# Kernel optimization log

Measured on AMD Instinct MI355X. Metric: run time of the kernel, lower is better.

The kernel has to match this reference:

```python
import jax, jax.numpy as jnp
import numpy as np

B, C, W, H = 4, 256, 64, 64
D = C // 8  # reduced query/key channels


def setup_inputs() -> dict:
    key = jax.random.key(0)
    k1, k2, k3, k4, k5 = jax.random.split(key, 5)
    return {
        "x": jax.random.normal(k1, (B, C, W, H), dtype=jnp.float32),
        "q_weight": jax.random.normal(k2, (D, C), dtype=jnp.float32) * 0.05,
        "k_weight": jax.random.normal(k3, (D, C), dtype=jnp.float32) * 0.05,
        "v_weight": jax.random.normal(k4, (C, C), dtype=jnp.float32) * 0.05,
        "gamma": jax.random.normal(k5, (1,), dtype=jnp.float32),
    }


def reference(x, q_weight, k_weight, v_weight, gamma):
    b, c, w, h = x.shape
    n = w * h
    xf = x.reshape(b, c, n)                       # (B, C, N)
    # 1x1 convs == channel matmuls
    q = jnp.einsum('dc,bcn->bdn', q_weight, xf)   # (B, D, N)
    k = jnp.einsum('dc,bcn->bdn', k_weight, xf)   # (B, D, N)
    v = jnp.einsum('oc,bcn->bon', v_weight, xf)   # (B, C, N)
    # energy[b, i, j] = <q[:, i], k[:, j]>  (unscaled, single head)
    energy = jnp.einsum('bdi,bdj->bij', q, k)     # (B, N, N)
    attn = jax.nn.softmax(energy, axis=-1)        # softmax over keys j
    # out[b, c, i] = sum_j v[b, c, j] * attn[b, i, j]
    out = jnp.einsum('bcj,bij->bci', v, attn)     # (B, C, N)
    out = out.reshape(b, c, w, h)
    return gamma[0] * out + x
```

## Files before the change

kernel.cpp:

```cpp
#include <hip/hip_runtime.h>
#include <math.h>

#define Bb 4
#define Cc 256
#define Nn 4096
#define Dd 32
#define XST 264

typedef __attribute__((ext_vector_type(8))) short bf16x8;
typedef __attribute__((ext_vector_type(4))) float f32x4;

__device__ __forceinline__ unsigned short f2bf(float x) {
    union { float f; unsigned u; } c; c.f = x;
    unsigned r = c.u + 0x7fffu + ((c.u >> 16) & 1u);
    return (unsigned short)(r >> 16);
}
__device__ __forceinline__ unsigned pk2(float a, float b) {
    return (unsigned)f2bf(a) | ((unsigned)f2bf(b) << 16);
}
__device__ __forceinline__ float fexp2(float x) {
#if __has_builtin(__builtin_amdgcn_exp2f)
    return __builtin_amdgcn_exp2f(x);
#else
    return __exp2f(x);
#endif
}
__device__ __forceinline__ void wg_barrier() {
    asm volatile("s_waitcnt lgkmcnt(0)\n\ts_barrier" ::: "memory");
}
template <int CTRL>
__device__ __forceinline__ float dppf(float v) {
    int iv = __builtin_bit_cast(int, v);
    return __builtin_bit_cast(float,
        __builtin_amdgcn_update_dpp(iv, iv, CTRL, 0xF, 0xF, false));
}
__device__ __forceinline__ float rowsum16(float v) {
    v += dppf<0xB1>(v);
    v += dppf<0x4E>(v);
    v += dppf<0x141>(v);
    v += dppf<0x140>(v);
    return v;
}

__global__ __launch_bounds__(256) void pack_w(
    const float* __restrict__ qw, const float* __restrict__ kw,
    const float* __restrict__ vw, short* __restrict__ wpk) {
    const int g = blockIdx.x * 256 + threadIdx.x;
    const int qd = g & 3, m = (g >> 2) & 15, kc = (g >> 6) & 7, ot = g >> 9;
    const int o = 16 * ot + m;
    const float* src;
    float scale = 1.0f;
    if (o < 32)      { src = qw + (size_t)o * Cc; scale = 1.44269504088896f; }
    else if (o < 64) { src = kw + (size_t)(o - 32) * Cc; }
    else             { src = vw + (size_t)(o - 64) * Cc; }
    const float* s8 = src + 32 * kc + 8 * qd;
    uint4 u;
    u.x = pk2(s8[0] * scale, s8[1] * scale);
    u.y = pk2(s8[2] * scale, s8[3] * scale);
    u.z = pk2(s8[4] * scale, s8[5] * scale);
    u.w = pk2(s8[6] * scale, s8[7] * scale);
    *(uint4*)(wpk + (size_t)g * 8) = u;
}

__global__ __launch_bounds__(256) void proj(
    const float* __restrict__ x, const short* __restrict__ wpk,
    short* __restrict__ q_t, short* __restrict__ k_t, short* __restrict__ v_b) {
    __shared__ alignas(16) short xs[32 * XST];
    const int b = blockIdx.z;
    const int n0 = blockIdx.x * 32;
    const int tid = threadIdx.x;
    const int w = tid >> 6;
    const int lane = tid & 63, qd = lane >> 4, m = lane & 15;

    {
        const int n = tid & 31, cg = tid >> 5;
        const float* xp = x + ((size_t)b * Cc + 32 * cg) * Nn + n0 + n;
        float xv[32];
#pragma unroll
        for (int i = 0; i < 32; ++i) xv[i] = xp[(size_t)i * Nn];
        short* row = xs + n * XST + 32 * cg;
#pragma unroll
        for (int u4 = 0; u4 < 4; ++u4)
            *(uint4*)(row + 8 * u4) = make_uint4(
                pk2(xv[8*u4+0], xv[8*u4+1]), pk2(xv[8*u4+2], xv[8*u4+3]),
                pk2(xv[8*u4+4], xv[8*u4+5]), pk2(xv[8*u4+6], xv[8*u4+7]));
    }
    __syncthreads();

    const int fslot = m * 4 + qd;
    f32x4 acc[5][2];
#pragma unroll
    for (int i = 0; i < 5; ++i)
#pragma unroll
        for (int nt = 0; nt < 2; ++nt) acc[i][nt] = (f32x4){0.f, 0.f, 0.f, 0.f};

    bf16x8 afc[5], afn[5];
#pragma unroll
    for (int i = 0; i < 5; ++i)
        afc[i] = *(const bf16x8*)(wpk + ((size_t)((4*i + w) * 8 + 0) * 64 + fslot) * 8);

    for (int kc = 0; kc < 8; ++kc) {
        if (kc < 7) {
#pragma unroll
            for (int i = 0; i < 5; ++i)
                afn[i] = *(const bf16x8*)(
                    wpk + ((size_t)((4*i + w) * 8 + kc + 1) * 64 + fslot) * 8);
        }
        const bf16x8 b0 = *(const bf16x8*)&xs[(     m) * XST + 32 * kc + 8 * qd];
        const bf16x8 b1 = *(const bf16x8*)&xs[(16 + m) * XST + 32 * kc + 8 * qd];
#pragma unroll
        for (int i = 0; i < 5; ++i)
            acc[i][0] = __builtin_amdgcn_mfma_f32_16x16x32_bf16(afc[i], b0, acc[i][0], 0, 0, 0);
#pragma unroll
        for (int i = 0; i < 5; ++i)
            acc[i][1] = __builtin_amdgcn_mfma_f32_16x16x32_bf16(afc[i], b1, acc[i][1], 0, 0, 0);
#pragma unroll
        for (int i = 0; i < 5; ++i) afc[i] = afn[i];
    }

#pragma unroll
    for (int i = 0; i < 5; ++i) {
        const int ot = 4 * i + w;
        if (ot < 4) {
            short* dst = (ot < 2 ? q_t : k_t) + (size_t)b * Nn * Dd;
            const int dbase = (ot & 1) * 16 + 4 * qd;
#pragma unroll
            for (int nt = 0; nt < 2; ++nt) {
                const f32x4 a = acc[i][nt];
                *(uint2*)(dst + (size_t)(n0 + 16 * nt + m) * Dd + dbase) =
                    make_uint2(pk2(a[0], a[1]), pk2(a[2], a[3]));
            }
        } else {
            const int ct = ot - 4;
            const int jt = n0 >> 6;
            const int b5 = (n0 >> 5) & 1;
            const size_t vbase =
                (((size_t)(b * 64 + jt) * 32 + ct * 2 + (m >> 3)) * 64
                 + ((m >> 1) & 3) * 16 + 4 * qd) * 8 + 4 * (m & 1) + 2 * b5;
#pragma unroll
            for (int rr = 0; rr < 4; ++rr) {
                const unsigned pv = pk2(acc[i][0][rr], acc[i][1][rr]);
                *(unsigned*)(v_b + vbase + rr * 8) = pv;
            }
        }
    }
}

__global__ __launch_bounds__(512) void attn(
    const float* __restrict__ x, const short* __restrict__ q_t,
    const short* __restrict__ k_t, const short* __restrict__ v_b,
    const float* __restrict__ gamma, float* __restrict__ out) {
    __shared__ alignas(16) char pool[34304];
    float* l_s = (float*)(pool + 33792);
    float* o_t = (float*)pool;

    const int fb  = blockIdx.x;
    const int xcd = fb & 7;
    const int b   = xcd >> 1;
    const int i0  = (((xcd & 1) << 5) | (fb >> 3)) << 6;
    const int tid = threadIdx.x;
    const int w = tid >> 6, lane = tid & 63;
    const int qd = lane >> 4, m = lane & 15;
    const int rt = w & 3, kh = w >> 2;

    const bf16x8 af = *(const bf16x8*)(
        q_t + ((size_t)b * Nn + i0 + 16 * rt + m) * Dd + 8 * qd);

    const short* kf = k_t + (size_t)b * Nn * Dd + (32 * kh + m) * Dd + 8 * qd;
    const short* vw = v_b + (size_t)b * (64 * 32 * 64 * 8) + (4 * w) * 512 + lane * 8;

    bf16x8 bkA0 = *(const bf16x8*)(kf);
    bf16x8 bkA1 = *(const bf16x8*)(kf + 512);
    bf16x8 bkB0 = *(const bf16x8*)(kf + 2048);
    bf16x8 bkB1 = *(const bf16x8*)(kf + 2560);
    bf16x8 vfA[2][2], vfB[2][2];
#pragma unroll
    for (int ct = 0; ct < 2; ++ct)
#pragma unroll
        for (int kc = 0; kc < 2; ++kc)
            vfA[ct][kc] = *(const bf16x8*)(vw + (2 * ct + kc) * 512);

    f32x4 oacc[4][2];
#pragma unroll
    for (int mt = 0; mt < 4; ++mt)
#pragma unroll
        for (int ct = 0; ct < 2; ++ct) oacc[mt][ct] = (f32x4){0.f, 0.f, 0.f, 0.f};
    float l_i[4] = {0.f, 0.f, 0.f, 0.f};

    const short* kpre = kf + 4096;
    const short* vpre = vw + 16384;

    for (int j2 = 0; j2 < 32; ++j2) {
        const bool pre = (j2 < 31);
        {
            short* ps = (short*)pool;
            const f32x4 s0 = __builtin_amdgcn_mfma_f32_16x16x32_bf16(
                af, bkA0, (f32x4){0.f, 0.f, 0.f, 0.f}, 0, 0, 0);
            const f32x4 s1 = __builtin_amdgcn_mfma_f32_16x16x32_bf16(
                af, bkA1, (f32x4){0.f, 0.f, 0.f, 0.f}, 0, 0, 0);
            if (pre) {
                bkA0 = *(const bf16x8*)(kpre);
                bkA1 = *(const bf16x8*)(kpre + 512);
            }
#pragma unroll
            for (int rr = 0; rr < 4; ++rr) {
                const float p0 = fexp2(s0[rr]);
                const float p1 = fexp2(s1[rr]);
                l_i[rr] += p0 + p1;
                *(unsigned*)&ps[(16 * rt + 4 * qd + rr) * 72 + 4 * m + 2 * kh] =
                    pk2(p0, p1);
            }
            wg_barrier();
#pragma unroll
            for (int ct = 0; ct < 2; ++ct)
#pragma unroll
                for (int kc = 0; kc < 2; ++kc)
                    vfB[ct][kc] = *(const bf16x8*)(vpre + (2 * ct + kc) * 512);
            __builtin_amdgcn_s_setprio(1);
#pragma unroll
            for (int kc = 0; kc < 2; ++kc) {
                bf16x8 pa[4];
#pragma unroll
                for (int mt = 0; mt < 4; ++mt)
                    pa[mt] = *(const bf16x8*)&ps[(16 * mt + m) * 72 + 32 * kc + 8 * qd];
#pragma unroll
                for (int ct = 0; ct < 2; ++ct)
#pragma unroll
                    for (int mt = 0; mt < 4; ++mt)
                        oacc[mt][ct] = __builtin_amdgcn_mfma_f32_16x16x32_bf16(
                            pa[mt], vfA[ct][kc], oacc[mt][ct], 0, 0, 0);
            }
            __builtin_amdgcn_s_setprio(0);
        }
        {
            short* ps = (short*)(pool + 9216);
            const f32x4 s0 = __builtin_amdgcn_mfma_f32_16x16x32_bf16(
                af, bkB0, (f32x4){0.f, 0.f, 0.f, 0.f}, 0, 0, 0);
            const f32x4 s1 = __builtin_amdgcn_mfma_f32_16x16x32_bf16(
                af, bkB1, (f32x4){0.f, 0.f, 0.f, 0.f}, 0, 0, 0);
            if (pre) {
                bkB0 = *(const bf16x8*)(kpre + 2048);
                bkB1 = *(const bf16x8*)(kpre + 2560);
            }
#pragma unroll
            for (int rr = 0; rr < 4; ++rr) {
                const float p0 = fexp2(s0[rr]);
                const float p1 = fexp2(s1[rr]);
                l_i[rr] += p0 + p1;
                *(unsigned*)&ps[(16 * rt + 4 * qd + rr) * 72 + 4 * m + 2 * kh] =
                    pk2(p0, p1);
            }
            wg_barrier();
            if (pre) {
#pragma unroll
                for (int ct = 0; ct < 2; ++ct)
#pragma unroll
                    for (int kc = 0; kc < 2; ++kc)
                        vfA[ct][kc] = *(const bf16x8*)(vpre + 16384 + (2 * ct + kc) * 512);
            }
            __builtin_amdgcn_s_setprio(1);
#pragma unroll
            for (int kc = 0; kc < 2; ++kc) {
                bf16x8 pa[4];
#pragma unroll
                for (int mt = 0; mt < 4; ++mt)
                    pa[mt] = *(const bf16x8*)&ps[(16 * mt + m) * 72 + 32 * kc + 8 * qd];
#pragma unroll
                for (int ct = 0; ct < 2; ++ct)
#pragma unroll
                    for (int mt = 0; mt < 4; ++mt)
                        oacc[mt][ct] = __builtin_amdgcn_mfma_f32_16x16x32_bf16(
                            pa[mt], vfB[ct][kc], oacc[mt][ct], 0, 0, 0);
            }
            __builtin_amdgcn_s_setprio(0);
        }
        kpre += 4096;
        vpre += 32768;
    }

#pragma unroll
    for (int rr = 0; rr < 4; ++rr) l_i[rr] = rowsum16(l_i[rr]);
    if (m == 0)
        *(f32x4*)&l_s[kh * 64 + 16 * rt + 4 * qd] =
            (f32x4){l_i[0], l_i[1], l_i[2], l_i[3]};
    __syncthreads();

    const float g = gamma[0];
    const int i = tid & 63, cg8 = tid >> 6;
    const float linv = 1.0f / (l_s[i] + l_s[64 + i]);
#pragma unroll
    for (int ps = 0; ps < 2; ++ps) {
        if (ps) __syncthreads();
#pragma unroll
        for (int mt = 0; mt < 4; ++mt)
#pragma unroll
            for (int rr = 0; rr < 4; ++rr)
                o_t[(16 * mt + 4 * qd + rr) * 132 + 16 * w + m] = oacc[mt][ps][rr];
        __syncthreads();
#pragma unroll
        for (int u = 0; u < 4; ++u) {
            const f32x4 v4 = *(const f32x4*)&o_t[i * 132 + 16 * cg8 + 4 * u];
#pragma unroll
            for (int e = 0; e < 4; ++e) {
                const int c = 32 * cg8 + 16 * ps + 4 * u + e;
                const size_t gidx = ((size_t)b * Cc + c) * Nn + i0 + i;
                out[gidx] = g * v4[e] * linv + x[gidx];
            }
        }
    }
}

extern "C" void kernel_launch(void* const* d_in, const int* in_sizes, int n_in,
                              void* d_out, int out_size, void* d_ws, size_t ws_size,
                              hipStream_t stream) {
    const float* x     = (const float*)d_in[0];
    const float* qw    = (const float*)d_in[1];
    const float* kw    = (const float*)d_in[2];
    const float* vw    = (const float*)d_in[3];
    const float* gamma = (const float*)d_in[4];
    float* out = (float*)d_out;

    short* q_t = (short*)d_ws;
    short* k_t = q_t + (size_t)Bb * Nn * Dd;
    short* v_b = k_t + (size_t)Bb * Nn * Dd;
    short* wpk = v_b + (size_t)Bb * Cc * Nn;

    pack_w<<<dim3(40), 256, 0, stream>>>(qw, kw, vw, wpk);
    proj<<<dim3(Nn / 32, 1, Bb), 256, 0, stream>>>(x, wpk, q_t, k_t, v_b);
    attn<<<dim3(256), 512, 0, stream>>>(x, q_t, k_t, v_b, gamma, out);
}
```

Before: 135.8 us.

## Split attention output channels across two blocks to double grid parallelism

The attention kernel now launches 512 blocks instead of 256. Each block handles 64 query rows and half of the 256 value channels, so each wave keeps one channel tile of accumulators instead of two. This halves per-block PV work and register use (launch bounds now request 4 blocks per SM), which should fill the 256 CUs better. In exchange, QK^T and the softmax exponentials are computed twice per query tile, and K is loaded by both halves.

```diff
diff --git a/kernel.cpp b/kernel.cpp
--- a/kernel.cpp
+++ b/kernel.cpp
@@ -146,7 +146,7 @@
     }
 }
 
-__global__ __launch_bounds__(512) void attn(
+__global__ __launch_bounds__(512, 4) void attn(
     const float* __restrict__ x, const short* __restrict__ q_t,
     const short* __restrict__ k_t, const short* __restrict__ v_b,
     const float* __restrict__ gamma, float* __restrict__ out) {
@@ -154,10 +154,11 @@
     float* l_s = (float*)(pool + 33792);
     float* o_t = (float*)pool;
 
-    const int fb  = blockIdx.x;
-    const int xcd = fb & 7;
-    const int b   = xcd >> 1;
-    const int i0  = (((xcd & 1) << 5) | (fb >> 3)) << 6;
+    const int fb   = blockIdx.x;
+    const int xcd  = fb & 7;
+    const int b    = xcd >> 1;
+    const int half = xcd & 1;
+    const int i0   = (fb >> 3) << 6;
     const int tid = threadIdx.x;
     const int w = tid >> 6, lane = tid & 63;
     const int qd = lane >> 4, m = lane & 15;
@@ -167,24 +168,21 @@
         q_t + ((size_t)b * Nn + i0 + 16 * rt + m) * Dd + 8 * qd);
 
     const short* kf = k_t + (size_t)b * Nn * Dd + (32 * kh + m) * Dd + 8 * qd;
-    const short* vw = v_b + (size_t)b * (64 * 32 * 64 * 8) + (4 * w) * 512 + lane * 8;
+    const short* vw = v_b + (size_t)b * (64 * 32 * 64 * 8)
+                    + (size_t)(16 * half + 2 * w) * 512 + lane * 8;
 
     bf16x8 bkA0 = *(const bf16x8*)(kf);
     bf16x8 bkA1 = *(const bf16x8*)(kf + 512);
     bf16x8 bkB0 = *(const bf16x8*)(kf + 2048);
     bf16x8 bkB1 = *(const bf16x8*)(kf + 2560);
-    bf16x8 vfA[2][2], vfB[2][2];
-#pragma unroll
-    for (int ct = 0; ct < 2; ++ct)
-#pragma unroll
-        for (int kc = 0; kc < 2; ++kc)
-            vfA[ct][kc] = *(const bf16x8*)(vw + (2 * ct + kc) * 512);
-
-    f32x4 oacc[4][2];
-#pragma unroll
-    for (int mt = 0; mt < 4; ++mt)
-#pragma unroll
-        for (int ct = 0; ct < 2; ++ct) oacc[mt][ct] = (f32x4){0.f, 0.f, 0.f, 0.f};
+    bf16x8 vfA[2], vfB[2];
+#pragma unroll
+    for (int kc = 0; kc < 2; ++kc)
+        vfA[kc] = *(const bf16x8*)(vw + kc * 512);
+
+    f32x4 oacc[4];
+#pragma unroll
+    for (int mt = 0; mt < 4; ++mt) oacc[mt] = (f32x4){0.f, 0.f, 0.f, 0.f};
     float l_i[4] = {0.f, 0.f, 0.f, 0.f};
 
     const short* kpre = kf + 4096;
@@ -212,10 +210,8 @@
             }
             wg_barrier();
 #pragma unroll
-            for (int ct = 0; ct < 2; ++ct)
-#pragma unroll
-                for (int kc = 0; kc < 2; ++kc)
-                    vfB[ct][kc] = *(const bf16x8*)(vpre + (2 * ct + kc) * 512);
+            for (int kc = 0; kc < 2; ++kc)
+                vfB[kc] = *(const bf16x8*)(vpre + kc * 512);
             __builtin_amdgcn_s_setprio(1);
 #pragma unroll
             for (int kc = 0; kc < 2; ++kc) {
@@ -224,11 +220,9 @@
                 for (int mt = 0; mt < 4; ++mt)
                     pa[mt] = *(const bf16x8*)&ps[(16 * mt + m) * 72 + 32 * kc + 8 * qd];
 #pragma unroll
-                for (int ct = 0; ct < 2; ++ct)
-#pragma unroll
-                    for (int mt = 0; mt < 4; ++mt)
-                        oacc[mt][ct] = __builtin_amdgcn_mfma_f32_16x16x32_bf16(
-                            pa[mt], vfA[ct][kc], oacc[mt][ct], 0, 0, 0);
+                for (int mt = 0; mt < 4; ++mt)
+                    oacc[mt] = __builtin_amdgcn_mfma_f32_16x16x32_bf16(
+                        pa[mt], vfA[kc], oacc[mt], 0, 0, 0);
             }
             __builtin_amdgcn_s_setprio(0);
         }
@@ -253,10 +247,8 @@
             wg_barrier();
             if (pre) {
 #pragma unroll
-                for (int ct = 0; ct < 2; ++ct)
-#pragma unroll
-                    for (int kc = 0; kc < 2; ++kc)
-                        vfA[ct][kc] = *(const bf16x8*)(vpre + 16384 + (2 * ct + kc) * 512);
+                for (int kc = 0; kc < 2; ++kc)
+                    vfA[kc] = *(const bf16x8*)(vpre + 16384 + kc * 512);
             }
             __builtin_amdgcn_s_setprio(1);
 #pragma unroll
@@ -266,11 +258,9 @@
                 for (int mt = 0; mt < 4; ++mt)
                     pa[mt] = *(const bf16x8*)&ps[(16 * mt + m) * 72 + 32 * kc + 8 * qd];
 #pragma unroll
-                for (int ct = 0; ct < 2; ++ct)
-#pragma unroll
-                    for (int mt = 0; mt < 4; ++mt)
-                        oacc[mt][ct] = __builtin_amdgcn_mfma_f32_16x16x32_bf16(
-                            pa[mt], vfB[ct][kc], oacc[mt][ct], 0, 0, 0);
+                for (int mt = 0; mt < 4; ++mt)
+                    oacc[mt] = __builtin_amdgcn_mfma_f32_16x16x32_bf16(
+                        pa[mt], vfB[kc], oacc[mt], 0, 0, 0);
             }
             __builtin_amdgcn_s_setprio(0);
         }
@@ -286,23 +276,21 @@
     __syncthreads();
 
     const float g = gamma[0];
-    const int i = tid & 63, cg8 = tid >> 6;
-    const float linv = 1.0f / (l_s[i] + l_s[64 + i]);
-#pragma unroll
-    for (int ps = 0; ps < 2; ++ps) {
-        if (ps) __syncthreads();
-#pragma unroll
-        for (int mt = 0; mt < 4; ++mt)
-#pragma unroll
-            for (int rr = 0; rr < 4; ++rr)
-                o_t[(16 * mt + 4 * qd + rr) * 132 + 16 * w + m] = oacc[mt][ps][rr];
-        __syncthreads();
+#pragma unroll
+    for (int mt = 0; mt < 4; ++mt)
+#pragma unroll
+        for (int rr = 0; rr < 4; ++rr)
+            o_t[(16 * mt + 4 * qd + rr) * 132 + 16 * w + m] = oacc[mt][rr];
+    __syncthreads();
+    {
+        const int i = tid & 63, cg8 = tid >> 6;
+        const float linv = 1.0f / (l_s[i] + l_s[64 + i]);
 #pragma unroll
         for (int u = 0; u < 4; ++u) {
             const f32x4 v4 = *(const f32x4*)&o_t[i * 132 + 16 * cg8 + 4 * u];
 #pragma unroll
             for (int e = 0; e < 4; ++e) {
-                const int c = 32 * cg8 + 16 * ps + 4 * u + e;
+                const int c = 128 * half + 16 * cg8 + 4 * u + e;
                 const size_t gidx = ((size_t)b * Cc + c) * Nn + i0 + i;
                 out[gidx] = g * v4[e] * linv + x[gidx];
             }
@@ -327,5 +315,5 @@
 
     pack_w<<<dim3(40), 256, 0, stream>>>(qw, kw, vw, wpk);
     proj<<<dim3(Nn / 32, 1, Bb), 256, 0, stream>>>(x, wpk, q_t, k_t, v_b);
-    attn<<<dim3(256), 512, 0, stream>>>(x, q_t, k_t, v_b, gamma, out);
-}
+    attn<<<dim3(512), 512, 0, stream>>>(x, q_t, k_t, v_b, gamma, out);
+}
```

Result: slower. 154.5 us (+13.8%).

## Software-pipeline attention loop so next tile's exp overlaps current PV MFMA

Applied to the files above, without the earlier changes.

Restructures the key-tile loop into a prologue, steady state and epilogue. The QK^T scores and exp/pack for tile j+1 are now computed while the PV MFMAs for tile j consume the other LDS buffer. The per-stage barrier count stays the same, but exp/VALU work is now interleaved with matrix work rather than serialised before it. The cost is more live registers, which may raise spills or pressure, and a subtler double-buffer ordering across the two LDS probability buffers.

```diff
diff --git a/kernel.cpp b/kernel.cpp
--- a/kernel.cpp
+++ b/kernel.cpp
@@ -153,6 +153,8 @@
     __shared__ alignas(16) char pool[34304];
     float* l_s = (float*)(pool + 33792);
     float* o_t = (float*)pool;
+    short* buf0 = (short*)pool;
+    short* buf1 = (short*)(pool + 9216);
 
     const int fb  = blockIdx.x;
     const int xcd = fb & 7;
@@ -187,95 +189,159 @@
         for (int ct = 0; ct < 2; ++ct) oacc[mt][ct] = (f32x4){0.f, 0.f, 0.f, 0.f};
     float l_i[4] = {0.f, 0.f, 0.f, 0.f};
 
-    const short* kpre = kf + 4096;
+    {
+        const f32x4 s0 = __builtin_amdgcn_mfma_f32_16x16x32_bf16(
+            af, bkA0, (f32x4){0.f, 0.f, 0.f, 0.f}, 0, 0, 0);
+        const f32x4 s1 = __builtin_amdgcn_mfma_f32_16x16x32_bf16(
+            af, bkA1, (f32x4){0.f, 0.f, 0.f, 0.f}, 0, 0, 0);
+        bkA0 = *(const bf16x8*)(kf + 4096);
+        bkA1 = *(const bf16x8*)(kf + 4096 + 512);
+#pragma unroll
+        for (int rr = 0; rr < 4; ++rr) {
+            const float p0 = fexp2(s0[rr]);
+            const float p1 = fexp2(s1[rr]);
+            l_i[rr] += p0 + p1;
+            *(unsigned*)&buf0[(16 * rt + 4 * qd + rr) * 72 + 4 * m + 2 * kh] =
+                pk2(p0, p1);
+        }
+        wg_barrier();
+    }
+
+    const short* kpre = kf + 3 * 2048;
     const short* vpre = vw + 16384;
 
-    for (int j2 = 0; j2 < 32; ++j2) {
-        const bool pre = (j2 < 31);
+    for (int j2 = 0; j2 < 31; ++j2) {
         {
-            short* ps = (short*)pool;
+            const f32x4 s0 = __builtin_amdgcn_mfma_f32_16x16x32_bf16(
+                af, bkB0, (f32x4){0.f, 0.f, 0.f, 0.f}, 0, 0, 0);
+            const f32x4 s1 = __builtin_amdgcn_mfma_f32_16x16x32_bf16(
+                af, bkB1, (f32x4){0.f, 0.f, 0.f, 0.f}, 0, 0, 0);
+            bkB0 = *(const bf16x8*)(kpre);
+            bkB1 = *(const bf16x8*)(kpre + 512);
+#pragma unroll
+            for (int ct = 0; ct < 2; ++ct)
+#pragma unroll
+                for (int kc = 0; kc < 2; ++kc)
+                    vfB[ct][kc] = *(const bf16x8*)(vpre + (2 * ct + kc) * 512);
+            __builtin_amdgcn_s_setprio(1);
+#pragma unroll
+            for (int kc = 0; kc < 2; ++kc) {
+                bf16x8 pa[4];
+#pragma unroll
+                for (int mt = 0; mt < 4; ++mt)
+                    pa[mt] = *(const bf16x8*)&buf0[(16 * mt + m) * 72 + 32 * kc + 8 * qd];
+#pragma unroll
+                for (int ct = 0; ct < 2; ++ct)
+#pragma unroll
+                    for (int mt = 0; mt < 4; ++mt)
+                        oacc[mt][ct] = __builtin_amdgcn_mfma_f32_16x16x32_bf16(
+                            pa[mt], vfA[ct][kc], oacc[mt][ct], 0, 0, 0);
+            }
+            __builtin_amdgcn_s_setprio(0);
+#pragma unroll
+            for (int rr = 0; rr < 4; ++rr) {
+                const float p0 = fexp2(s0[rr]);
+                const float p1 = fexp2(s1[rr]);
+                l_i[rr] += p0 + p1;
+                *(unsigned*)&buf1[(16 * rt + 4 * qd + rr) * 72 + 4 * m + 2 * kh] =
+                    pk2(p0, p1);
+            }
+            wg_barrier();
+        }
+        {
             const f32x4 s0 = __builtin_amdgcn_mfma_f32_16x16x32_bf16(
                 af, bkA0, (f32x4){0.f, 0.f, 0.f, 0.f}, 0, 0, 0);
             const f32x4 s1 = __builtin_amdgcn_mfma_f32_16x16x32_bf16(
                 af, bkA1, (f32x4){0.f, 0.f, 0.f, 0.f}, 0, 0, 0);
-            if (pre) {
-                bkA0 = *(const bf16x8*)(kpre);
-                bkA1 = *(const bf16x8*)(kpre + 512);
-            }
+            if (j2 < 30) {
+                bkA0 = *(const bf16x8*)(kpre + 2048);
+                bkA1 = *(const bf16x8*)(kpre + 2560);
+            }
+#pragma unroll
+            for (int ct = 0; ct < 2; ++ct)
+#pragma unroll
+                for (int kc = 0; kc < 2; ++kc)
+                    vfA[ct][kc] = *(const bf16x8*)(vpre + 16384 + (2 * ct + kc) * 512);
+            __builtin_amdgcn_s_setprio(1);
+#pragma unroll
+            for (int kc = 0; kc < 2; ++kc) {
+                bf16x8 pa[4];
+#pragma unroll
+                for (int mt = 0; mt < 4; ++mt)
+                    pa[mt] = *(const bf16x8*)&buf1[(16 * mt + m) * 72 + 32 * kc + 8 * qd];
+#pragma unroll
+                for (int ct = 0; ct < 2; ++ct)
+#pragma unroll
+                    for (int mt = 0; mt < 4; ++mt)
+                        oacc[mt][ct] = __builtin_amdgcn_mfma_f32_16x16x32_bf16(
+                            pa[mt], vfB[ct][kc], oacc[mt][ct], 0, 0, 0);
+            }
+            __builtin_amdgcn_s_setprio(0);
 #pragma unroll
             for (int rr = 0; rr < 4; ++rr) {
                 const float p0 = fexp2(s0[rr]);
                 const float p1 = fexp2(s1[rr]);
                 l_i[rr] += p0 + p1;
-                *(unsigned*)&ps[(16 * rt + 4 * qd + rr) * 72 + 4 * m + 2 * kh] =
+                *(unsigned*)&buf0[(16 * rt + 4 * qd + rr) * 72 + 4 * m + 2 * kh] =
                     pk2(p0, p1);
             }
             wg_barrier();
-#pragma unroll
-            for (int ct = 0; ct < 2; ++ct)
-#pragma unroll
-                for (int kc = 0; kc < 2; ++kc)
-                    vfB[ct][kc] = *(const bf16x8*)(vpre + (2 * ct + kc) * 512);
-            __builtin_amdgcn_s_setprio(1);
-#pragma unroll
-            for (int kc = 0; kc < 2; ++kc) {
-                bf16x8 pa[4];
-#pragma unroll
-                for (int mt = 0; mt < 4; ++mt)
-                    pa[mt] = *(const bf16x8*)&ps[(16 * mt + m) * 72 + 32 * kc + 8 * qd];
-#pragma unroll
-                for (int ct = 0; ct < 2; ++ct)
-#pragma unroll
-                    for (int mt = 0; mt < 4; ++mt)
-                        oacc[mt][ct] = __builtin_amdgcn_mfma_f32_16x16x32_bf16(
-                            pa[mt], vfA[ct][kc], oacc[mt][ct], 0, 0, 0);
-            }
-            __builtin_amdgcn_s_setprio(0);
-        }
-        {
-            short* ps = (short*)(pool + 9216);
-            const f32x4 s0 = __builtin_amdgcn_mfma_f32_16x16x32_bf16(
-                af, bkB0, (f32x4){0.f, 0.f, 0.f, 0.f}, 0, 0, 0);
-            const f32x4 s1 = __builtin_amdgcn_mfma_f32_16x16x32_bf16(
-                af, bkB1, (f32x4){0.f, 0.f, 0.f, 0.f}, 0, 0, 0);
-            if (pre) {
-                bkB0 = *(const bf16x8*)(kpre + 2048);
-                bkB1 = *(const bf16x8*)(kpre + 2560);
-            }
-#pragma unroll
-            for (int rr = 0; rr < 4; ++rr) {
-                const float p0 = fexp2(s0[rr]);
-                const float p1 = fexp2(s1[rr]);
-                l_i[rr] += p0 + p1;
-                *(unsigned*)&ps[(16 * rt + 4 * qd + rr) * 72 + 4 * m + 2 * kh] =
-                    pk2(p0, p1);
-            }
-            wg_barrier();
-            if (pre) {
-#pragma unroll
-                for (int ct = 0; ct < 2; ++ct)
-#pragma unroll
-                    for (int kc = 0; kc < 2; ++kc)
-                        vfA[ct][kc] = *(const bf16x8*)(vpre + 16384 + (2 * ct + kc) * 512);
-            }
-            __builtin_amdgcn_s_setprio(1);
-#pragma unroll
-            for (int kc = 0; kc < 2; ++kc) {
-                bf16x8 pa[4];
-#pragma unroll
-                for (int mt = 0; mt < 4; ++mt)
-                    pa[mt] = *(const bf16x8*)&ps[(16 * mt + m) * 72 + 32 * kc + 8 * qd];
-#pragma unroll
-                for (int ct = 0; ct < 2; ++ct)
-#pragma unroll
-                    for (int mt = 0; mt < 4; ++mt)
-                        oacc[mt][ct] = __builtin_amdgcn_mfma_f32_16x16x32_bf16(
-                            pa[mt], vfB[ct][kc], oacc[mt][ct], 0, 0, 0);
-            }
-            __builtin_amdgcn_s_setprio(0);
         }
         kpre += 4096;
         vpre += 32768;
+    }
+
+    {
+        const f32x4 s0 = __builtin_amdgcn_mfma_f32_16x16x32_bf16(
+            af, bkB0, (f32x4){0.f, 0.f, 0.f, 0.f}, 0, 0, 0);
+        const f32x4 s1 = __builtin_amdgcn_mfma_f32_16x16x32_bf16(
+            af, bkB1, (f32x4){0.f, 0.f, 0.f, 0.f}, 0, 0, 0);
+#pragma unroll
+        for (int ct = 0; ct < 2; ++ct)
+#pragma unroll
+            for (int kc = 0; kc < 2; ++kc)
+                vfB[ct][kc] = *(const bf16x8*)(vpre + (2 * ct + kc) * 512);
+        __builtin_amdgcn_s_setprio(1);
+#pragma unroll
+        for (int kc = 0; kc < 2; ++kc) {
+            bf16x8 pa[4];
+#pragma unroll
+            for (int mt = 0; mt < 4; ++mt)
+                pa[mt] = *(const bf16x8*)&buf0[(16 * mt + m) * 72 + 32 * kc + 8 * qd];
+#pragma unroll
+            for (int ct = 0; ct < 2; ++ct)
+#pragma unroll
+                for (int mt = 0; mt < 4; ++mt)
+                    oacc[mt][ct] = __builtin_amdgcn_mfma_f32_16x16x32_bf16(
+                        pa[mt], vfA[ct][kc], oacc[mt][ct], 0, 0, 0);
+        }
+        __builtin_amdgcn_s_setprio(0);
+#pragma unroll
+        for (int rr = 0; rr < 4; ++rr) {
+            const float p0 = fexp2(s0[rr]);
+            const float p1 = fexp2(s1[rr]);
+            l_i[rr] += p0 + p1;
+            *(unsigned*)&buf1[(16 * rt + 4 * qd + rr) * 72 + 4 * m + 2 * kh] =
+                pk2(p0, p1);
+        }
+        wg_barrier();
+    }
+    {
+        __builtin_amdgcn_s_setprio(1);
+#pragma unroll
+        for (int kc = 0; kc < 2; ++kc) {
+            bf16x8 pa[4];
+#pragma unroll
+            for (int mt = 0; mt < 4; ++mt)
+                pa[mt] = *(const bf16x8*)&buf1[(16 * mt + m) * 72 + 32 * kc + 8 * qd];
+#pragma unroll
+            for (int ct = 0; ct < 2; ++ct)
+#pragma unroll
+                for (int mt = 0; mt < 4; ++mt)
+                    oacc[mt][ct] = __builtin_amdgcn_mfma_f32_16x16x32_bf16(
+                        pa[mt], vfB[ct][kc], oacc[mt][ct], 0, 0, 0);
+        }
+        __builtin_amdgcn_s_setprio(0);
     }
 
 #pragma unroll
```

Measured after the change: 134.9 us. No clear change (-0.7%).

## Split attention workgroup into producer and consumer waves with ping-pong buffers

Applied to the files above, without the earlier changes.

Warp-specializes the attention kernel: waves 0-3 compute QK^T scores, exponentials and row sums into LDS, while waves 4-7 load V and run the PV MFMAs on the previous buffer. This double-buffered software pipeline is meant to overlap exp/score work with the PV matrix multiplies instead of having every wave do both serially. In exchange, consumer waves hold 16 accumulators plus 16 V fragments, which raises register pressure, and producer waves may become the bottleneck. The LDS footprint and the epilogue layout are adjusted to match.

```diff
diff --git a/kernel.cpp b/kernel.cpp
--- a/kernel.cpp
+++ b/kernel.cpp
@@ -146,13 +146,57 @@
     }
 }
 
+__device__ __forceinline__ void produce(
+    const bf16x8 af, bf16x8 bk[4], const short* kpre, bool pre,
+    short* psbuf, float* l_i, int w, int qd, int m) {
+    f32x4 s[4];
+#pragma unroll
+    for (int nt = 0; nt < 4; ++nt)
+        s[nt] = __builtin_amdgcn_mfma_f32_16x16x32_bf16(
+            af, bk[nt], (f32x4){0.f, 0.f, 0.f, 0.f}, 0, 0, 0);
+    if (pre) {
+#pragma unroll
+        for (int nt = 0; nt < 4; ++nt)
+            bk[nt] = *(const bf16x8*)(kpre + nt * 512);
+    }
+#pragma unroll
+    for (int rr = 0; rr < 4; ++rr) {
+        const float p0 = fexp2(s[0][rr]);
+        const float p1 = fexp2(s[1][rr]);
+        const float p2 = fexp2(s[2][rr]);
+        const float p3 = fexp2(s[3][rr]);
+        l_i[rr] += (p0 + p1) + (p2 + p3);
+        *(uint2*)&psbuf[(16 * w + 4 * qd + rr) * 72 + 4 * m] =
+            make_uint2(pk2(p0, p1), pk2(p2, p3));
+    }
+}
+
+__device__ __forceinline__ void consume(
+    const short* psbuf, const bf16x8* vf, f32x4* oacc, int qd, int m) {
+#pragma unroll
+    for (int kc = 0; kc < 2; ++kc) {
+        bf16x8 pa[4];
+#pragma unroll
+        for (int mt = 0; mt < 4; ++mt)
+            pa[mt] = *(const bf16x8*)&psbuf[(16 * mt + m) * 72 + 32 * kc + 8 * qd];
+#pragma unroll
+        for (int ct = 0; ct < 4; ++ct)
+#pragma unroll
+            for (int mt = 0; mt < 4; ++mt)
+                oacc[4 * mt + ct] = __builtin_amdgcn_mfma_f32_16x16x32_bf16(
+                    pa[mt], vf[2 * ct + kc], oacc[4 * mt + ct], 0, 0, 0);
+    }
+}
+
 __global__ __launch_bounds__(512) void attn(
     const float* __restrict__ x, const short* __restrict__ q_t,
     const short* __restrict__ k_t, const short* __restrict__ v_b,
     const float* __restrict__ gamma, float* __restrict__ out) {
-    __shared__ alignas(16) char pool[34304];
-    float* l_s = (float*)(pool + 33792);
-    float* o_t = (float*)pool;
+    __shared__ alignas(16) char pool[18688];
+    short* buf0 = (short*)pool;
+    short* buf1 = (short*)(pool + 9216);
+    float* l_s  = (float*)(pool + 18432);
+    float* o_t  = (float*)pool;
 
     const int fb  = blockIdx.x;
     const int xcd = fb & 7;
@@ -161,148 +205,114 @@
     const int tid = threadIdx.x;
     const int w = tid >> 6, lane = tid & 63;
     const int qd = lane >> 4, m = lane & 15;
-    const int rt = w & 3, kh = w >> 2;
-
-    const bf16x8 af = *(const bf16x8*)(
-        q_t + ((size_t)b * Nn + i0 + 16 * rt + m) * Dd + 8 * qd);
-
-    const short* kf = k_t + (size_t)b * Nn * Dd + (32 * kh + m) * Dd + 8 * qd;
-    const short* vw = v_b + (size_t)b * (64 * 32 * 64 * 8) + (4 * w) * 512 + lane * 8;
-
-    bf16x8 bkA0 = *(const bf16x8*)(kf);
-    bf16x8 bkA1 = *(const bf16x8*)(kf + 512);
-    bf16x8 bkB0 = *(const bf16x8*)(kf + 2048);
-    bf16x8 bkB1 = *(const bf16x8*)(kf + 2560);
-    bf16x8 vfA[2][2], vfB[2][2];
-#pragma unroll
-    for (int ct = 0; ct < 2; ++ct)
-#pragma unroll
-        for (int kc = 0; kc < 2; ++kc)
-            vfA[ct][kc] = *(const bf16x8*)(vw + (2 * ct + kc) * 512);
-
-    f32x4 oacc[4][2];
-#pragma unroll
-    for (int mt = 0; mt < 4; ++mt)
-#pragma unroll
-        for (int ct = 0; ct < 2; ++ct) oacc[mt][ct] = (f32x4){0.f, 0.f, 0.f, 0.f};
+    const bool isProd = (w < 4);
+
+    bf16x8 af;
+    bf16x8 bkA[4], bkB[4];
+    bf16x8 vfA[8], vfB[8];
+    f32x4 oacc[16];
     float l_i[4] = {0.f, 0.f, 0.f, 0.f};
 
-    const short* kpre = kf + 4096;
+    const short* kf = k_t + (size_t)b * Nn * Dd + m * Dd + 8 * qd;
+    const short* vw = v_b + (size_t)b * (64 * 32 * 64 * 8)
+                    + (size_t)(8 * (w - 4)) * 512 + lane * 8;
+
+    if (isProd) {
+        af = *(const bf16x8*)(q_t + ((size_t)b * Nn + i0 + 16 * w + m) * Dd + 8 * qd);
+#pragma unroll
+        for (int nt = 0; nt < 4; ++nt)
+            bkA[nt] = *(const bf16x8*)(kf + nt * 512);
+        produce(af, bkA, kf + 4096, true, buf0, l_i, w, qd, m);
+#pragma unroll
+        for (int nt = 0; nt < 4; ++nt)
+            bkB[nt] = *(const bf16x8*)(kf + 2048 + nt * 512);
+    } else {
+#pragma unroll
+        for (int i = 0; i < 8; ++i)
+            vfA[i] = *(const bf16x8*)(vw + i * 512);
+#pragma unroll
+        for (int i = 0; i < 16; ++i) oacc[i] = (f32x4){0.f, 0.f, 0.f, 0.f};
+    }
+    wg_barrier();
+
+    const short* kpre = kf + 3 * 2048;
     const short* vpre = vw + 16384;
 
-    for (int j2 = 0; j2 < 32; ++j2) {
-        const bool pre = (j2 < 31);
-        {
-            short* ps = (short*)pool;
-            const f32x4 s0 = __builtin_amdgcn_mfma_f32_16x16x32_bf16(
-                af, bkA0, (f32x4){0.f, 0.f, 0.f, 0.f}, 0, 0, 0);
-            const f32x4 s1 = __builtin_amdgcn_mfma_f32_16x16x32_bf16(
-                af, bkA1, (f32x4){0.f, 0.f, 0.f, 0.f}, 0, 0, 0);
-            if (pre) {
-                bkA0 = *(const bf16x8*)(kpre);
-                bkA1 = *(const bf16x8*)(kpre + 512);
-            }
-#pragma unroll
-            for (int rr = 0; rr < 4; ++rr) {
-                const float p0 = fexp2(s0[rr]);
-                const float p1 = fexp2(s1[rr]);
-                l_i[rr] += p0 + p1;
-                *(unsigned*)&ps[(16 * rt + 4 * qd + rr) * 72 + 4 * m + 2 * kh] =
-                    pk2(p0, p1);
-            }
-            wg_barrier();
-#pragma unroll
-            for (int ct = 0; ct < 2; ++ct)
-#pragma unroll
-                for (int kc = 0; kc < 2; ++kc)
-                    vfB[ct][kc] = *(const bf16x8*)(vpre + (2 * ct + kc) * 512);
+    for (int j2 = 0; j2 < 31; ++j2) {
+        if (isProd) {
+            produce(af, bkB, kpre, true, buf1, l_i, w, qd, m);
+        } else {
+#pragma unroll
+            for (int i = 0; i < 8; ++i)
+                vfB[i] = *(const bf16x8*)(vpre + i * 512);
             __builtin_amdgcn_s_setprio(1);
-#pragma unroll
-            for (int kc = 0; kc < 2; ++kc) {
-                bf16x8 pa[4];
-#pragma unroll
-                for (int mt = 0; mt < 4; ++mt)
-                    pa[mt] = *(const bf16x8*)&ps[(16 * mt + m) * 72 + 32 * kc + 8 * qd];
-#pragma unroll
-                for (int ct = 0; ct < 2; ++ct)
-#pragma unroll
-                    for (int mt = 0; mt < 4; ++mt)
-                        oacc[mt][ct] = __builtin_amdgcn_mfma_f32_16x16x32_bf16(
-                            pa[mt], vfA[ct][kc], oacc[mt][ct], 0, 0, 0);
-            }
+            consume(buf0, vfA, oacc, qd, m);
             __builtin_amdgcn_s_setprio(0);
         }
-        {
-            short* ps = (short*)(pool + 9216);
-            const f32x4 s0 = __builtin_amdgcn_mfma_f32_16x16x32_bf16(
-                af, bkB0, (f32x4){0.f, 0.f, 0.f, 0.f}, 0, 0, 0);
-            const f32x4 s1 = __builtin_amdgcn_mfma_f32_16x16x32_bf16(
-                af, bkB1, (f32x4){0.f, 0.f, 0.f, 0.f}, 0, 0, 0);
-            if (pre) {
-                bkB0 = *(const bf16x8*)(kpre + 2048);
-                bkB1 = *(const bf16x8*)(kpre + 2560);
-            }
-#pragma unroll
-            for (int rr = 0; rr < 4; ++rr) {
-                const float p0 = fexp2(s0[rr]);
-                const float p1 = fexp2(s1[rr]);
-                l_i[rr] += p0 + p1;
-                *(unsigned*)&ps[(16 * rt + 4 * qd + rr) * 72 + 4 * m + 2 * kh] =
-                    pk2(p0, p1);
-            }
-            wg_barrier();
-            if (pre) {
-#pragma unroll
-                for (int ct = 0; ct < 2; ++ct)
-#pragma unroll
-                    for (int kc = 0; kc < 2; ++kc)
-                        vfA[ct][kc] = *(const bf16x8*)(vpre + 16384 + (2 * ct + kc) * 512);
-            }
+        wg_barrier();
+        if (isProd) {
+            produce(af, bkA, kpre + 2048, j2 < 30, buf0, l_i, w, qd, m);
+        } else {
+#pragma unroll
+            for (int i = 0; i < 8; ++i)
+                vfA[i] = *(const bf16x8*)(vpre + 16384 + i * 512);
             __builtin_amdgcn_s_setprio(1);
-#pragma unroll
-            for (int kc = 0; kc < 2; ++kc) {
-                bf16x8 pa[4];
-#pragma unroll
-                for (int mt = 0; mt < 4; ++mt)
-                    pa[mt] = *(const bf16x8*)&ps[(16 * mt + m) * 72 + 32 * kc + 8 * qd];
-#pragma unroll
-                for (int ct = 0; ct < 2; ++ct)
-#pragma unroll
-                    for (int mt = 0; mt < 4; ++mt)
-                        oacc[mt][ct] = __builtin_amdgcn_mfma_f32_16x16x32_bf16(
-                            pa[mt], vfB[ct][kc], oacc[mt][ct], 0, 0, 0);
-            }
+            consume(buf1, vfB, oacc, qd, m);
             __builtin_amdgcn_s_setprio(0);
         }
+        wg_barrier();
         kpre += 4096;
         vpre += 32768;
     }
 
-#pragma unroll
-    for (int rr = 0; rr < 4; ++rr) l_i[rr] = rowsum16(l_i[rr]);
-    if (m == 0)
-        *(f32x4*)&l_s[kh * 64 + 16 * rt + 4 * qd] =
-            (f32x4){l_i[0], l_i[1], l_i[2], l_i[3]};
+    if (isProd) {
+        produce(af, bkB, kf, false, buf1, l_i, w, qd, m);
+    } else {
+#pragma unroll
+        for (int i = 0; i < 8; ++i)
+            vfB[i] = *(const bf16x8*)(vpre + i * 512);
+        __builtin_amdgcn_s_setprio(1);
+        consume(buf0, vfA, oacc, qd, m);
+        __builtin_amdgcn_s_setprio(0);
+    }
+    wg_barrier();
+    if (!isProd) {
+        __builtin_amdgcn_s_setprio(1);
+        consume(buf1, vfB, oacc, qd, m);
+        __builtin_amdgcn_s_setprio(0);
+    }
+
+    if (isProd) {
+#pragma unroll
+        for (int rr = 0; rr < 4; ++rr) l_i[rr] = rowsum16(l_i[rr]);
+        if (m == 0)
+            *(f32x4*)&l_s[16 * w + 4 * qd] = (f32x4){l_i[0], l_i[1], l_i[2], l_i[3]};
+    }
     __syncthreads();
 
     const float g = gamma[0];
     const int i = tid & 63, cg8 = tid >> 6;
-    const float linv = 1.0f / (l_s[i] + l_s[64 + i]);
-#pragma unroll
-    for (int ps = 0; ps < 2; ++ps) {
+    const float linv = 1.0f / l_s[i];
+#pragma unroll
+    for (int ps = 0; ps < 4; ++ps) {
         if (ps) __syncthreads();
-#pragma unroll
-        for (int mt = 0; mt < 4; ++mt)
-#pragma unroll
-            for (int rr = 0; rr < 4; ++rr)
-                o_t[(16 * mt + 4 * qd + rr) * 132 + 16 * w + m] = oacc[mt][ps][rr];
+        if (!isProd) {
+            const int wp = w - 4;
+#pragma unroll
+            for (int mt = 0; mt < 4; ++mt)
+#pragma unroll
+                for (int rr = 0; rr < 4; ++rr)
+                    o_t[(16 * mt + 4 * qd + rr) * 68 + 16 * wp + m] =
+                        oacc[4 * mt + ps][rr];
+        }
         __syncthreads();
 #pragma unroll
-        for (int u = 0; u < 4; ++u) {
-            const f32x4 v4 = *(const f32x4*)&o_t[i * 132 + 16 * cg8 + 4 * u];
+        for (int u = 0; u < 2; ++u) {
+            const f32x4 v4 = *(const f32x4*)&o_t[i * 68 + 8 * cg8 + 4 * u];
 #pragma unroll
             for (int e = 0; e < 4; ++e) {
-                const int c = 32 * cg8 + 16 * ps + 4 * u + e;
+                const int cc = 8 * cg8 + 4 * u + e;
+                const int c = 64 * (cc >> 4) + 16 * ps + (cc & 15);
                 const size_t gidx = ((size_t)b * Cc + c) * Nn + i0 + i;
                 out[gidx] = g * v4[e] * linv + x[gidx];
             }
```

New measurement: 429.1 us. +215.9%, slower.
